# Kernel optimization log

Measured on AMD Instinct MI355X. Metric: run time of the kernel, lower is better.

The kernel has to match this reference:

```python
import jax, jax.numpy as jnp
import numpy as np
from jax import lax

B, T, N, D = 4, 12, 1024, 128
C_FRONT = 78           # front/back channel split used by the mixup
X_LAST = T // 2 - 1    # static row index of the last (only effective) mixup call
BS_ST = 6              # block_size of mixup_region_ST
SIGMA = 10.0
LN_EPS = 1e-5


def _mixup_region_ST(graph, y):
    """Faithful jax port of mixup_region_ST(graph_front, x=X_LAST, y, 6, sigma=10).
    graph: [T, N, C_FRONT] float; y: traced int scalar."""
    T_, N_, C_ = graph.shape
    x = X_LAST  # static python int
    y_start = jnp.maximum(y - BS_ST, 0)
    y_end = jnp.minimum(y + 2 * BS_ST, N_)

    # temporal gaussian mix of column y over rows [0, x), written at (x, y)
    xs = jnp.arange(x, dtype=graph.dtype)
    w = jnp.exp(-((xs - (x - 1.0)) ** 2) / (2.0 * SIGMA ** 2))
    w = w / w.sum()
    target = graph[:x, y, :]                      # [x, C]
    mixed_value = (w[:, None] * target).sum(0)    # [C]
    g = lax.dynamic_update_slice(graph, mixed_value[None, None, :], (x, y, 0))

    def mix_write(g_, bs, maxj):
        # average blocks g_[:, j*bs:(j+1)*bs, :] for j in [y_start//bs, y_end//bs)
        j0 = y_start // bs
        j1 = y_end // bs
        jj = jnp.arange(maxj)
        mask = (jj < (j1 - j0)).astype(g_.dtype)              # [maxj]
        cols = jnp.clip((j0 + jj)[:, None] * bs + jnp.arange(bs)[None, :], 0, N_ - 1)
        blocks = g_[:, cols, :]                               # [T, maxj, bs, C]
        mixed = (blocks * mask[None, :, None, None]).sum(1) / (j1 - j0).astype(g_.dtype)
        # torch writes mixed_region.to(torch.uint8) into a float tensor
        mixed = lax.stop_gradient(mixed.astype(jnp.uint8).astype(g_.dtype))
        return lax.dynamic_update_slice(g_, mixed, (0, y, 0))

    # torch resets block_size to 1 when y_end > w - block_size
    return lax.cond(y_end > N_ - BS_ST,
                    lambda g_: mix_write(g_, 1, 3 * BS_ST),
                    lambda g_: mix_write(g_, BS_ST, 4),
                    g)


def _forward(inp, adapt_G, xff_w, xff_b, ff1_w, ff1_b, ff2_w, ff2_b, ln_w, ln_b):
    x_ = inp @ xff_w.T + xff_b                       # [B,T,N,3D]
    q, k, v = jnp.split(x_, 3, axis=-1)
    e = jnp.einsum('btnd,btmd->btnm', q, k) / (D ** 0.5)
    e = e @ adapt_G                                  # [B,T,N,N]
    attn = jax.nn.softmax(e, axis=-1)
    attn_det = lax.stop_gradient(attn)               # self.attention_maps = attn.detach()

    def process(attn_b, val_b):                      # [T,N,N], [T,N,D]
        front = val_b[..., :C_FRONT]
        back = val_b[..., C_FRONT:]
        col_sums = attn_b.sum(axis=1)                # [T, N]
        _, idx = lax.top_k(-col_sums, 2)             # 2 smallest per row, ascending
        # only the last loop iteration's mixup survives in the original code
        y = idx[X_LAST, 1]
        return jnp.concatenate([_mixup_region_ST(front, y), back], axis=-1)

    new_value = jax.vmap(process)(attn_det, v)       # [B,T,N,D]
    vi = attn @ new_value                            # [B,T,N,D]
    h = jax.nn.gelu(vi @ ff1_w.T + ff1_b, approximate=False)
    h = h @ ff2_w.T + ff2_b
    out = h + inp
    mu = out.mean(-1, keepdims=True)
    var = ((out - mu) ** 2).mean(-1, keepdims=True)
    return (out - mu) / jnp.sqrt(var + LN_EPS) * ln_w + ln_b


def setup_inputs() -> dict:
    key = jax.random.key(0)
    ks = jax.random.split(key, 6)
    s = 0.02
    return {
        'input': jax.random.normal(ks[0], (B, T, N, D), jnp.float32),
        'adapt_G': jax.random.normal(ks[1], (N, N), jnp.float32) / np.float32(np.sqrt(N)),
        'xff_w': jax.random.normal(ks[2], (3 * D, D), jnp.float32) * s,
        'xff_b': jnp.zeros((3 * D,), jnp.float32),
        'ff1_w': jax.random.normal(ks[3], (D, D), jnp.float32) * s,
        'ff1_b': jnp.zeros((D,), jnp.float32),
        'ff2_w': jax.random.normal(ks[4], (D, D), jnp.float32) * s,
        'ff2_b': jnp.zeros((D,), jnp.float32),
        'ln_w': jnp.ones((D,), jnp.float32),
        'ln_b': jnp.zeros((D,), jnp.float32),
    }


def reference(input, adapt_G, xff_w, xff_b, ff1_w, ff1_b, ff2_w, ff2_b, ln_w, ln_b):
    return _forward(input, adapt_G, xff_w, xff_b, ff1_w, ff1_b, ff2_w, ff2_b, ln_w, ln_b)
```

## Files before the change

kernel.cpp:

```cpp
#include <hip/hip_runtime.h>
#include <hip/hip_bf16.h>

typedef __attribute__((ext_vector_type(8))) short bf16x8;
typedef __attribute__((ext_vector_type(4))) float f32x4;
typedef unsigned long long ull;

#define MFMA(a,b,c) __builtin_amdgcn_mfma_f32_16x16x32_bf16((a),(b),(c),0,0,0)
#define VMCNT(N) asm volatile("s_waitcnt vmcnt(%0)" :: "i"(N) : "memory")

__device__ __forceinline__ short f2bs(float f){
  union { float f; unsigned u; } x; x.f = f;
  unsigned r = (x.u + 0x7fffu + ((x.u >> 16) & 1u)) >> 16;
  return (short)r;
}
__device__ __forceinline__ float bs2f(short s){
  union { unsigned u; float f; } x; x.u = ((unsigned)(unsigned short)s) << 16;
  return x.f;
}

__device__ __forceinline__ void gl2lds16(const void* g, void* l){
  __builtin_amdgcn_global_load_lds((const __attribute__((address_space(1))) void*)g,
                                   (__attribute__((address_space(3))) void*)l, 16, 0, 0);
}

__device__ __forceinline__ void merge2(ull& a1, ull& a2, ull b1, ull b2){
  ull n1 = min(a1, b1);
  ull n2 = min(max(a1, b1), min(a2, b2));
  a1 = n1; a2 = n2;
}

__global__ void conv_kernel(const float* xffw, const float* w1, const float* w2,
                            short* wqkv_b, short* w1_b, short* w2_b){
  int i = blockIdx.x*blockDim.x + threadIdx.x;
  int stride = gridDim.x*blockDim.x;
  for (int idx = i; idx < 384*128; idx += stride) wqkv_b[idx] = f2bs(xffw[idx]);
  for (int idx = i; idx < 128*128; idx += stride) w1_b[idx] = f2bs(w1[idx]);
  for (int idx = i; idx < 128*128; idx += stride) w2_b[idx] = f2bs(w2[idx]);
}

__global__ __launch_bounds__(256) void gtrans_kernel(const float* __restrict__ G,
                                                     short* __restrict__ gt){
  __shared__ float tile[32][33];
  int bx = blockIdx.x & 31;
  int by = blockIdx.x >> 5;
  int tx = threadIdx.x & 31, ty = threadIdx.x >> 5;
  #pragma unroll
  for (int j=0;j<4;j++){
    int n = by*32 + ty + j*8;
    tile[ty+j*8][tx] = G[(size_t)n*1024 + bx*32 + tx];
  }
  __syncthreads();
  #pragma unroll
  for (int j=0;j<4;j++){
    int m = bx*32 + ty + j*8;
    gt[(size_t)m*1024 + by*32 + tx] = f2bs(tile[tx][ty+j*8]);
  }
}

__global__ __launch_bounds__(256,3) void qkv_kernel(const float* __restrict__ inp,
                                                  const short* __restrict__ wqkv,
                                                  const float* __restrict__ bias,
                                                  short* __restrict__ q, short* __restrict__ kT,
                                                  short* __restrict__ nvt){
  __shared__ __align__(16) char smem[49152];
  int w = threadIdx.x >> 6, lane = threadIdx.x & 63;
  int lr = lane & 15, lg = lane >> 4;
  int r0 = blockIdx.x*64;
  int bt = blockIdx.x >> 4;
  int n0 = r0 & 1023;
  int rw = r0 + w*16;
  bf16x8 a[4];
  #pragma unroll
  for (int kc=0;kc<4;kc++){
    const float* ar = inp + (size_t)(rw+lr)*128 + kc*32 + lg*8;
    float4 f0 = *(const float4*)ar;
    float4 f1 = *(const float4*)(ar+4);
    bf16x8 t;
    t[0]=f2bs(f0.x); t[1]=f2bs(f0.y); t[2]=f2bs(f0.z); t[3]=f2bs(f0.w);
    t[4]=f2bs(f1.x); t[5]=f2bs(f1.y); t[6]=f2bs(f1.z); t[7]=f2bs(f1.w);
    a[kc]=t;
  }
  auto stageW = [&](int buf, int kc){
    #pragma unroll
    for (int t=0;t<6;t++){
      int r = (w*6+t)*16 + (lane>>2);
      int s = (lane&3) ^ ((r>>1)&3);
      gl2lds16(wqkv + (size_t)r*128 + kc*32 + s*8,
               smem + buf*24576 + (w*6+t)*1024);
    }
  };
  f32x4 acc[24];
  #pragma unroll
  for (int j=0;j<24;j++) acc[j] = f32x4{0.f,0.f,0.f,0.f};
  stageW(0, 0);
  int cur = 0;
  for (int kc=0; kc<4; kc++){
    if (kc < 3) { stageW(cur^1, kc+1); VMCNT(6); } else { VMCNT(0); }
    __builtin_amdgcn_s_barrier();
    __builtin_amdgcn_sched_barrier(0);
    const char* wb = smem + cur*24576;
    #pragma unroll
    for (int jt=0;jt<24;jt++){
      int j = jt*16 + lr;
      bf16x8 b = *(const bf16x8*)(wb + (size_t)j*64 + ((lg ^ ((lr>>1)&3))*16));
      acc[jt] = MFMA(a[kc], b, acc[jt]);
    }
    __builtin_amdgcn_s_barrier();
    cur ^= 1;
  }
  #pragma unroll
  for (int jt=0;jt<8;jt++){
    float bj = bias[jt*16+lr];
    #pragma unroll
    for (int rr=0;rr<4;rr++)
      q[(size_t)(rw + lg*4 + rr)*128 + jt*16 + lr] = f2bs(acc[jt][rr] + bj);
  }
  __syncthreads();
  short (*tb)[72] = (short(*)[72])smem;
  #pragma unroll
  for (int jt=8;jt<16;jt++){
    int d = (jt-8)*16 + lr;
    float bj = bias[jt*16+lr];
    #pragma unroll
    for (int rr=0;rr<4;rr++) tb[d][w*16 + lg*4 + rr] = f2bs(acc[jt][rr] + bj);
  }
  __syncthreads();
  #pragma unroll
  for (int it=0;it<4;it++){
    int idx = it*256 + threadIdx.x;
    int row = idx >> 3, c8 = (idx & 7)*8;
    *(bf16x8*)(kT + ((size_t)bt*128 + row)*1024 + n0 + c8) = *(const bf16x8*)&tb[row][c8];
  }
  __syncthreads();
  #pragma unroll
  for (int jt=16;jt<24;jt++){
    int c = (jt-16)*16 + lr;
    float bj = bias[jt*16+lr];
    #pragma unroll
    for (int rr=0;rr<4;rr++) tb[c][w*16 + lg*4 + rr] = f2bs(acc[jt][rr] + bj);
  }
  __syncthreads();
  #pragma unroll
  for (int it=0;it<4;it++){
    int idx = it*256 + threadIdx.x;
    int row = idx >> 3, c8 = (idx & 7)*8;
    *(bf16x8*)(nvt + ((size_t)bt*128 + row)*1024 + n0 + c8) = *(const bf16x8*)&tb[row][c8];
  }
}

__global__ __launch_bounds__(256,3) void kg_kernel(const short* __restrict__ gt,
                                                   const short* __restrict__ kT,
                                                   short* __restrict__ kgt){
  __shared__ __align__(16) short gtl[2][64*64];
  __shared__ __align__(16) short ktl[2][128*64];
  int lb = (blockIdx.x & 7)*96 + (blockIdx.x >> 3);
  int bt = lb >> 4;
  int mt = lb & 15;
  int w = threadIdx.x>>6, lane = threadIdx.x&63, lr = lane&15, lg = lane>>4;
  int mblk = mt*64;
  const short* kbase = kT + (size_t)bt*128*1024;
  auto stage = [&](int b, int nc){
    int n0 = nc*64;
    #pragma unroll
    for (int t=0;t<2;t++){
      int row = w*16 + t*8 + (lane>>3);
      int cswz = ((lane&7)*16) ^ ((row&7)<<4);
      gl2lds16(gt + (size_t)(mblk+row)*1024 + n0 + (cswz>>1),
               (char*)gtl[b] + w*2048 + t*1024);
    }
    #pragma unroll
    for (int t=0;t<4;t++){
      int row = w*32 + t*8 + (lane>>3);
      int cswz = ((lane&7)*16) ^ ((row&7)<<4);
      gl2lds16(kbase + (size_t)row*1024 + n0 + (cswz>>1),
               (char*)ktl[b] + w*4096 + t*1024);
    }
  };
  f32x4 acc[8];
  #pragma unroll
  for (int i=0;i<8;i++) acc[i] = f32x4{0.f,0.f,0.f,0.f};
  stage(0, 0);
  int cur = 0;
  for (int nc=0; nc<16; nc++){
    if (nc < 15) { stage(cur^1, nc+1); VMCNT(6); } else { VMCNT(0); }
    __builtin_amdgcn_s_barrier();
    __builtin_amdgcn_sched_barrier(0);
    #pragma unroll
    for (int ks=0;ks<2;ks++){
      int arl = w*16 + lr;
      int acb = ks*64 + lg*16;
      bf16x8 af = *(const bf16x8*)((const char*)gtl[cur] + arl*128 + (acb ^ ((arl&7)<<4)));
      #pragma unroll
      for (int dt=0;dt<8;dt++){
        int brl = dt*16 + lr;
        bf16x8 bf = *(const bf16x8*)((const char*)ktl[cur] + brl*128 + (acb ^ ((brl&7)<<4)));
        acc[dt] = MFMA(af, bf, acc[dt]);
      }
    }
    __builtin_amdgcn_s_barrier();
    cur ^= 1;
  }
  const float SCALE = 0.08838834764831845f;
  int m = mblk + w*16 + lg*4;
  #pragma unroll
  for (int dt=0;dt<8;dt++){
    #pragma unroll
    for (int rr=0;rr<4;rr++){
      kgt[((size_t)(bt*1024 + m + rr))*128 + dt*16 + lr] = f2bs(acc[dt][rr]*SCALE);
    }
  }
}

__global__ __launch_bounds__(256,3) void fused_kernel(const short* __restrict__ q,
                                                      const short* __restrict__ kgt,
                                                      const short* __restrict__ nvt,
                                                      float* __restrict__ zbuf,
                                                      float* __restrict__ cspart,
                                                      short* __restrict__ vib){
  __shared__ __align__(16) short kgl[64*128];
  __shared__ __align__(16) short nvl[128*64];
  __shared__ __align__(16) short p_lds[4][16][68];
  __shared__ float csb[4][64];
  int lb = (blockIdx.x & 7)*96 + (blockIdx.x >> 3);
  int bt = lb >> 4;
  int rblk = lb & 15;
  int w = threadIdx.x>>6, lane = threadIdx.x&63, lr = lane&15, lg = lane>>4;
  int r0 = rblk*64 + w*16;
  const short* qrow = q + ((size_t)(bt*1024 + r0 + lr))*128;
  bf16x8 a[4];
  #pragma unroll
  for (int kc=0;kc<4;kc++) a[kc] = *(const bf16x8*)(qrow + kc*32 + lg*8);
  const short* kgb = kgt + (size_t)bt*1024*128;
  const short* nvb = nvt + (size_t)bt*128*1024;
  auto stage_kg = [&](int mc){
    int m0 = mc*64;
    #pragma unroll
    for (int t=0;t<4;t++){
      int row = w*16 + t*4 + (lane>>4);
      int cswz = ((lane&15)*16) ^ ((row&7)<<4);
      gl2lds16(kgb + (size_t)(m0+row)*128 + (cswz>>1),
               (char*)kgl + w*4096 + t*1024);
    }
  };
  auto stage_nv = [&](int mc){
    int m0 = mc*64;
    #pragma unroll
    for (int t=0;t<4;t++){
      int row = w*32 + t*8 + (lane>>3);
      int cswz = ((lane&7)*16) ^ ((row&7)<<4);
      gl2lds16(nvb + (size_t)row*1024 + m0 + (cswz>>1),
               (char*)nvl + w*4096 + t*1024);
    }
  };
  f32x4 acc[8];
  #pragma unroll
  for (int i=0;i<8;i++) acc[i] = f32x4{0.f,0.f,0.f,0.f};
  float zacc[4] = {0.f,0.f,0.f,0.f};
  for (int mc=0; mc<16; mc++){
    stage_kg(mc);
    stage_nv(mc);
    __syncthreads();
    #pragma unroll
    for (int s=0;s<4;s++){
      f32x4 e = f32x4{0.f,0.f,0.f,0.f};
      #pragma unroll
      for (int kc=0;kc<4;kc++){
        int rl = s*16 + lr;
        int cb = kc*64 + lg*16;
        bf16x8 kb = *(const bf16x8*)((const char*)kgl + rl*256 + (cb ^ ((rl&7)<<4)));
        e = MFMA(a[kc], kb, e);
      }
      #pragma unroll
      for (int rr=0;rr<4;rr++){
        float p = __expf(fminf(e[rr], 60.f));
        zacc[rr] += p;
        p_lds[w][lg*4+rr][s*16+lr] = f2bs(p);
      }
    }
    bf16x8 pa0 = *(const bf16x8*)&p_lds[w][lr][lg*8];
    bf16x8 pa1 = *(const bf16x8*)&p_lds[w][lr][32+lg*8];
    #pragma unroll
    for (int ct=0; ct<8; ct++){
      int c = ct*16 + lr;
      int mb0 = lg*16;
      int mb1 = 64 + lg*16;
      bf16x8 nb0 = *(const bf16x8*)((const char*)nvl + c*128 + (mb0 ^ ((c&7)<<4)));
      bf16x8 nb1 = *(const bf16x8*)((const char*)nvl + c*128 + (mb1 ^ ((c&7)<<4)));
      acc[ct] = MFMA(pa0, nb0, acc[ct]);
      acc[ct] = MFMA(pa1, nb1, acc[ct]);
    }
    __syncthreads();
  }
  #pragma unroll
  for (int d=1;d<16;d<<=1){
    #pragma unroll
    for (int rr=0;rr<4;rr++) zacc[rr] += __shfl_xor(zacc[rr], d, 64);
  }
  if (lr==0){
    #pragma unroll
    for (int rr=0;rr<4;rr++) zbuf[(size_t)bt*1024 + r0 + lg*4 + rr] = zacc[rr];
  }
  float inv[4];
  #pragma unroll
  for (int rr=0;rr<4;rr++) inv[rr] = 1.0f/zacc[rr];
  #pragma unroll
  for (int ct=0;ct<8;ct++){
    #pragma unroll
    for (int rr=0;rr<4;rr++){
      vib[((size_t)(bt*1024 + r0 + lg*4 + rr))*128 + ct*16 + lr] = f2bs(acc[ct][rr]*inv[rr]);
    }
  }
  int t5 = bt % 12, b = bt / 12;
  if (t5 == 5){
    for (int mc=0; mc<16; mc++){
      stage_kg(mc);
      __syncthreads();
      int m0 = mc*64;
      float cs[4];
      #pragma unroll
      for (int s=0;s<4;s++){
        f32x4 e = f32x4{0.f,0.f,0.f,0.f};
        #pragma unroll
        for (int kc=0;kc<4;kc++){
          int rl = s*16 + lr;
          int cb = kc*64 + lg*16;
          bf16x8 kb = *(const bf16x8*)((const char*)kgl + rl*256 + (cb ^ ((rl&7)<<4)));
          e = MFMA(a[kc], kb, e);
        }
        float c = 0.f;
        #pragma unroll
        for (int rr=0;rr<4;rr++) c += __expf(fminf(e[rr],60.f))*inv[rr];
        c += __shfl_xor(c, 16, 64);
        c += __shfl_xor(c, 32, 64);
        cs[s] = c;
      }
      if (lg==0){
        #pragma unroll
        for (int s=0;s<4;s++) csb[w][s*16+lr] = cs[s];
      }
      __syncthreads();
      if (w==0){
        int j = lane;
        float tot = csb[0][j]+csb[1][j]+csb[2][j]+csb[3][j];
        cspart[((size_t)(b*16 + rblk))*1024 + m0 + j] = tot;
      }
    }
  }
}

__global__ __launch_bounds__(256) void top2_kernel(const float* __restrict__ cspart,
                                                   int* __restrict__ yidx){
  __shared__ ull s1[4], s2[4];
  int b = blockIdx.x;
  ull b1 = ~0ull, b2 = ~0ull;
  #pragma unroll
  for (int j=0;j<4;j++){
    int col = j*256 + threadIdx.x;
    float s = 0.f;
    #pragma unroll
    for (int blk=0;blk<16;blk++) s += cspart[((size_t)(b*16 + blk))*1024 + col];
    union { float f; unsigned u; } cv; cv.f = s;
    ull key = ((ull)cv.u << 32) | (unsigned)col;
    merge2(b1, b2, key, ~0ull);
  }
  #pragma unroll
  for (int d=1;d<64;d<<=1){
    ull o1 = __shfl_xor(b1, d, 64);
    ull o2 = __shfl_xor(b2, d, 64);
    merge2(b1, b2, o1, o2);
  }
  int w = threadIdx.x >> 6;
  if ((threadIdx.x & 63) == 0){ s1[w] = b1; s2[w] = b2; }
  __syncthreads();
  if (threadIdx.x == 0){
    ull r1 = s1[0], r2 = s2[0];
    merge2(r1, r2, s1[1], s2[1]);
    merge2(r1, r2, s1[2], s2[2]);
    merge2(r1, r2, s1[3], s2[3]);
    yidx[b] = (int)(r2 & 0xffffffffu);
  }
}

__global__ void nvfixA_kernel(const short* __restrict__ nvt, const int* __restrict__ yidx,
                              float* __restrict__ mixres){
  int bt = blockIdx.x; int b = bt/12, t = bt%12;
  int y = yidx[b];
  int y_start = max(y-6, 0), y_end = min(y+12, 1024);
  int bs, j0, cnt;
  if (y_end > 1024-6){ bs = 1; j0 = y_start; cnt = y_end - y_start; }
  else { bs = 6; j0 = y_start/6; cnt = y_end/6 - j0; }
  int items = bs*78;
  int idx = threadIdx.x;
  if (idx >= items) return;
  int i = idx / 78, c = idx % 78;
  const short* nvb = nvt + (size_t)bt*128*1024;
  float acc = 0.f;
  for (int jj=0;jj<cnt;jj++){
    int col = (j0+jj)*bs + i;
    float gv;
    if (t == 5 && col == y){
      float wsum = 0.f, mv = 0.f;
      #pragma unroll
      for (int tp=0;tp<5;tp++){
        float d = (float)tp - 4.0f;
        float w = __expf(-d*d/200.0f);
        wsum += w;
        mv += w * bs2f(nvt[((size_t)(b*12+tp)*128 + c)*1024 + y]);
      }
      gv = mv / wsum;
    } else {
      gv = bs2f(nvb[(size_t)c*1024 + col]);
    }
    acc += gv;
  }
  mixres[((size_t)bt*6 + i)*78 + c] = acc / (float)cnt;
}

__global__ __launch_bounds__(256) void corr_kernel(const short* __restrict__ q,
                                                   const short* __restrict__ kgt,
                                                   const short* __restrict__ nvt,
                                                   const float* __restrict__ mixres,
                                                   const float* __restrict__ zbuf,
                                                   const int* __restrict__ yidx,
                                                   short* __restrict__ vib){
  __shared__ __align__(16) short kcol[6][128];
  __shared__ float delta[6][78];
  int bt = blockIdx.x >> 2;
  int rc = blockIdx.x & 3;
  int b = bt/12;
  int y = yidx[b];
  int y_end = min(y+12, 1024);
  int bs = (y_end > 1024-6) ? 1 : 6;
  for (int idx = threadIdx.x; idx < 6*128; idx += 256){
    int i = idx >> 7, d = idx & 127;
    kcol[i][d] = (i < bs) ? kgt[((size_t)(bt*1024 + y + i))*128 + d] : (short)0;
  }
  for (int idx = threadIdx.x; idx < 6*78; idx += 256){
    int i = idx / 78, c = idx % 78;
    float dv = 0.f;
    if (i < bs){
      float avg = mixres[((size_t)bt*6 + i)*78 + c];
      int ti = (int)avg;
      unsigned char u = (unsigned char)ti;
      dv = (float)u - bs2f(nvt[((size_t)bt*128 + c)*1024 + (y+i)]);
    }
    delta[i][c] = dv;
  }
  __syncthreads();
  int r = rc*256 + threadIdx.x;
  const short* qr = q + ((size_t)(bt*1024 + r))*128;
  float e[6] = {0.f,0.f,0.f,0.f,0.f,0.f};
  for (int d0 = 0; d0 < 128; d0 += 8){
    bf16x8 qv = *(const bf16x8*)(qr + d0);
    #pragma unroll
    for (int j=0;j<8;j++){
      float qf = bs2f(qv[j]);
      #pragma unroll
      for (int i=0;i<6;i++) e[i] += qf * bs2f(kcol[i][d0+j]);
    }
  }
  float invz = 1.0f / zbuf[(size_t)bt*1024 + r];
  float p[6];
  #pragma unroll
  for (int i=0;i<6;i++) p[i] = (i < bs) ? __expf(fminf(e[i],60.f))*invz : 0.f;
  short* vr = vib + ((size_t)(bt*1024 + r))*128;
  for (int c=0;c<78;c++){
    float dsum = 0.f;
    #pragma unroll
    for (int i=0;i<6;i++) dsum += p[i]*delta[i][c];
    vr[c] = f2bs(bs2f(vr[c]) + dsum);
  }
}

__global__ __launch_bounds__(256,3) void ffn_kernel(const short* __restrict__ vib,
                                                  const float* __restrict__ inp,
                                                  const short* __restrict__ w1b,
                                                  const short* __restrict__ w2b,
                                                  const float* __restrict__ b1,
                                                  const float* __restrict__ b2,
                                                  const float* __restrict__ lnw,
                                                  const float* __restrict__ lnb,
                                                  float* __restrict__ out){
  __shared__ __align__(16) short wl[128*128];
  __shared__ __align__(16) short h_lds[4][16][72];
  int w = threadIdx.x>>6, lane = threadIdx.x&63, lr = lane&15, lg = lane>>4;
  int r0 = blockIdx.x*64 + w*16;
  auto stageW = [&](const short* src){
    #pragma unroll
    for (int t=0;t<8;t++){
      int r = (w*8+t)*4 + (lane>>4);
      int s = (lane&15) ^ (r&7);
      gl2lds16(src + (size_t)r*128 + s*8, (char*)wl + (w*8+t)*1024);
    }
  };
  stageW(w1b);
  bf16x8 a[4];
  #pragma unroll
  for (int kc=0;kc<4;kc++) a[kc] = *(const bf16x8*)(vib + (size_t)(r0+lr)*128 + kc*32 + lg*8);
  __syncthreads();
  f32x4 acc[8];
  #pragma unroll
  for (int i=0;i<8;i++) acc[i] = f32x4{0.f,0.f,0.f,0.f};
  #pragma unroll
  for (int kc=0;kc<4;kc++){
    #pragma unroll
    for (int jt=0;jt<8;jt++){
      bf16x8 b = *(const bf16x8*)((const char*)wl + (size_t)(jt*16+lr)*256 + (((kc*4+lg) ^ (lr&7))*16));
      acc[jt] = MFMA(a[kc], b, acc[jt]);
    }
  }
  #pragma unroll
  for (int jt=0;jt<8;jt++){
    float bj = b1[jt*16+lr];
    #pragma unroll
    for (int rr=0;rr<4;rr++){
      float x = acc[jt][rr] + bj;
      float g = 0.5f*x*(1.0f + erff(x*0.70710678118654752f));
      h_lds[w][lg*4+rr][jt*16+lr] = f2bs(g);
    }
  }
  __syncthreads();
  stageW(w2b);
  bf16x8 ha[4];
  #pragma unroll
  for (int kc=0;kc<4;kc++) ha[kc] = *(const bf16x8*)&h_lds[w][lr][kc*32 + lg*8];
  __syncthreads();
  f32x4 acc2[8];
  #pragma unroll
  for (int i=0;i<8;i++) acc2[i] = f32x4{0.f,0.f,0.f,0.f};
  #pragma unroll
  for (int kc=0;kc<4;kc++){
    #pragma unroll
    for (int jt=0;jt<8;jt++){
      bf16x8 b = *(const bf16x8*)((const char*)wl + (size_t)(jt*16+lr)*256 + (((kc*4+lg) ^ (lr&7))*16));
      acc2[jt] = MFMA(ha[kc], b, acc2[jt]);
    }
  }
  float xv[8][4];
  #pragma unroll
  for (int jt=0;jt<8;jt++){
    float bj = b2[jt*16+lr];
    #pragma unroll
    for (int rr=0;rr<4;rr++){
      xv[jt][rr] = acc2[jt][rr] + bj + inp[(size_t)(r0 + lg*4 + rr)*128 + jt*16 + lr];
    }
  }
  float mu[4], rstd[4];
  #pragma unroll
  for (int rr=0;rr<4;rr++){
    float s = 0.f;
    #pragma unroll
    for (int jt=0;jt<8;jt++) s += xv[jt][rr];
    #pragma unroll
    for (int m=1;m<16;m<<=1) s += __shfl_xor(s, m, 64);
    mu[rr] = s * (1.0f/128.0f);
  }
  #pragma unroll
  for (int rr=0;rr<4;rr++){
    float s = 0.f;
    #pragma unroll
    for (int jt=0;jt<8;jt++){ float d = xv[jt][rr]-mu[rr]; s += d*d; }
    #pragma unroll
    for (int m=1;m<16;m<<=1) s += __shfl_xor(s, m, 64);
    rstd[rr] = rsqrtf(s * (1.0f/128.0f) + 1e-5f);
  }
  #pragma unroll
  for (int jt=0;jt<8;jt++){
    int col = jt*16 + lr;
    float lw = lnw[col], lb = lnb[col];
    #pragma unroll
    for (int rr=0;rr<4;rr++){
      out[(size_t)(r0 + lg*4 + rr)*128 + col] = (xv[jt][rr]-mu[rr])*rstd[rr]*lw + lb;
    }
  }
}

extern "C" void kernel_launch(void* const* d_in, const int* in_sizes, int n_in,
                              void* d_out, int out_size, void* d_ws, size_t ws_size,
                              hipStream_t stream) {
  (void)in_sizes; (void)n_in; (void)out_size;
  const float* inp  = (const float*)d_in[0];
  const float* G    = (const float*)d_in[1];
  const float* xffw = (const float*)d_in[2];
  const float* xffb = (const float*)d_in[3];
  const float* w1   = (const float*)d_in[4];
  const float* b1   = (const float*)d_in[5];
  const float* w2   = (const float*)d_in[6];
  const float* b2   = (const float*)d_in[7];
  const float* lnw  = (const float*)d_in[8];
  const float* lnb  = (const float*)d_in[9];
  float* out = (float*)d_out;
  char* ws = (char*)d_ws;

  size_t off = 0;
  auto take = [&](size_t bytes)->char*{ char* p = ws + off; off += (bytes + 255) & ~(size_t)255; return p; };
  short* wqkv_b = (short*)take(384*128*2);
  short* gt_b   = (short*)take((size_t)1024*1024*2);
  short* w1_b   = (short*)take(128*128*2);
  short* w2_b   = (short*)take(128*128*2);
  short* qb     = (short*)take((size_t)48*1024*128*2);
  short* kTb    = (short*)take((size_t)48*128*1024*2);
  short* nvt    = (short*)take((size_t)48*128*1024*2);
  short* kgt    = (short*)take((size_t)48*1024*128*2);
  float* zbuf   = (float*)take((size_t)48*1024*4);
  float* cspart = (float*)take((size_t)4*16*1024*4);
  int*   yidx   = (int*)take(256);
  float* mixres = (float*)take((size_t)48*6*78*4);
  short* vibuf  = (short*)take((size_t)48*1024*128*2);
  if (off > ws_size) return;

  conv_kernel<<<dim3(32), dim3(256), 0, stream>>>(xffw, w1, w2, wqkv_b, w1_b, w2_b);
  gtrans_kernel<<<dim3(1024), dim3(256), 0, stream>>>(G, gt_b);
  qkv_kernel<<<dim3(768), dim3(256), 0, stream>>>(inp, wqkv_b, xffb, qb, kTb, nvt);
  kg_kernel<<<dim3(768), dim3(256), 0, stream>>>(gt_b, kTb, kgt);
  fused_kernel<<<dim3(768), dim3(256), 0, stream>>>(qb, kgt, nvt, zbuf, cspart, vibuf);
  top2_kernel<<<dim3(4), dim3(256), 0, stream>>>(cspart, yidx);
  nvfixA_kernel<<<dim3(48), dim3(512), 0, stream>>>(nvt, yidx, mixres);
  corr_kernel<<<dim3(192), dim3(256), 0, stream>>>(qb, kgt, nvt, mixres, zbuf, yidx, vibuf);
  ffn_kernel<<<dim3(768), dim3(256), 0, stream>>>(vibuf, inp, w1_b, w2_b, b1, b2, lnw, lnb, out);
}
```

Baseline: 160.2 us.

## Prefetch next K/V tiles in fused attention and offload column sums via stored probabilities

The fused attention loop now prefetches the next kg tile during the softmax phase and the next nv tile during the PV MFMA phase, using explicit vmcnt waits and raw barriers instead of a synchronous load then __syncthreads. The second pass over K for the t==5 slices, which recomputed exp scores to build column sums, is removed. Instead those blocks write their bf16 probability tiles to a buffer, and a new colsum kernel reduces them with 1/z normalisation before top2. This removes the serialised tail on 64 of the 768 blocks, at the cost of an extra launch, an 8MB write and read, and bf16 rounding of the column sums.

```diff
diff --git a/kernel.cpp b/kernel.cpp
--- a/kernel.cpp
+++ b/kernel.cpp
@@ -215,17 +215,18 @@
                                                       const short* __restrict__ kgt,
                                                       const short* __restrict__ nvt,
                                                       float* __restrict__ zbuf,
-                                                      float* __restrict__ cspart,
+                                                      short* __restrict__ pbuf,
                                                       short* __restrict__ vib){
   __shared__ __align__(16) short kgl[64*128];
   __shared__ __align__(16) short nvl[128*64];
-  __shared__ __align__(16) short p_lds[4][16][68];
-  __shared__ float csb[4][64];
+  __shared__ __align__(16) short p_lds[4][16][72];
   int lb = (blockIdx.x & 7)*96 + (blockIdx.x >> 3);
   int bt = lb >> 4;
   int rblk = lb & 15;
   int w = threadIdx.x>>6, lane = threadIdx.x&63, lr = lane&15, lg = lane>>4;
   int r0 = rblk*64 + w*16;
+  bool is5 = (bt % 12) == 5;
+  int bq = bt / 12;
   const short* qrow = q + ((size_t)(bt*1024 + r0 + lr))*128;
   bf16x8 a[4];
   #pragma unroll
@@ -256,10 +257,13 @@
   #pragma unroll
   for (int i=0;i<8;i++) acc[i] = f32x4{0.f,0.f,0.f,0.f};
   float zacc[4] = {0.f,0.f,0.f,0.f};
+  stage_kg(0);
+  stage_nv(0);
+  VMCNT(0);
+  __builtin_amdgcn_s_barrier();
+  __builtin_amdgcn_sched_barrier(0);
   for (int mc=0; mc<16; mc++){
-    stage_kg(mc);
-    stage_nv(mc);
-    __syncthreads();
+    int m0 = mc*64;
     #pragma unroll
     for (int s=0;s<4;s++){
       f32x4 e = f32x4{0.f,0.f,0.f,0.f};
@@ -277,6 +281,11 @@
         p_lds[w][lg*4+rr][s*16+lr] = f2bs(p);
       }
     }
+    __builtin_amdgcn_s_barrier();
+    if (mc < 15) stage_kg(mc+1);
+    if (mc < 15) { VMCNT(4); } else { VMCNT(0); }
+    __builtin_amdgcn_s_barrier();
+    __builtin_amdgcn_sched_barrier(0);
     bf16x8 pa0 = *(const bf16x8*)&p_lds[w][lr][lg*8];
     bf16x8 pa1 = *(const bf16x8*)&p_lds[w][lr][32+lg*8];
     #pragma unroll
@@ -289,7 +298,19 @@
       acc[ct] = MFMA(pa0, nb0, acc[ct]);
       acc[ct] = MFMA(pa1, nb1, acc[ct]);
     }
-    __syncthreads();
+    if (is5){
+      #pragma unroll
+      for (int tt=0; tt<4; tt++){
+        int row = tt*4 + (lane>>4);
+        int m = (lane&15)*4;
+        ull v = *(const ull*)&p_lds[w][row][m];
+        *(ull*)(pbuf + ((size_t)bq*1024 + r0 + row)*1024 + m0 + m) = v;
+      }
+    }
+    __builtin_amdgcn_s_barrier();
+    if (mc < 15) { stage_nv(mc+1); VMCNT(4); } else { VMCNT(0); }
+    __builtin_amdgcn_s_barrier();
+    __builtin_amdgcn_sched_barrier(0);
   }
   #pragma unroll
   for (int d=1;d<16;d<<=1){
@@ -310,45 +331,31 @@
       vib[((size_t)(bt*1024 + r0 + lg*4 + rr))*128 + ct*16 + lr] = f2bs(acc[ct][rr]*inv[rr]);
     }
   }
-  int t5 = bt % 12, b = bt / 12;
-  if (t5 == 5){
-    for (int mc=0; mc<16; mc++){
-      stage_kg(mc);
-      __syncthreads();
-      int m0 = mc*64;
-      float cs[4];
-      #pragma unroll
-      for (int s=0;s<4;s++){
-        f32x4 e = f32x4{0.f,0.f,0.f,0.f};
-        #pragma unroll
-        for (int kc=0;kc<4;kc++){
-          int rl = s*16 + lr;
-          int cb = kc*64 + lg*16;
-          bf16x8 kb = *(const bf16x8*)((const char*)kgl + rl*256 + (cb ^ ((rl&7)<<4)));
-          e = MFMA(a[kc], kb, e);
-        }
-        float c = 0.f;
-        #pragma unroll
-        for (int rr=0;rr<4;rr++) c += __expf(fminf(e[rr],60.f))*inv[rr];
-        c += __shfl_xor(c, 16, 64);
-        c += __shfl_xor(c, 32, 64);
-        cs[s] = c;
-      }
-      if (lg==0){
-        #pragma unroll
-        for (int s=0;s<4;s++) csb[w][s*16+lr] = cs[s];
-      }
-      __syncthreads();
-      if (w==0){
-        int j = lane;
-        float tot = csb[0][j]+csb[1][j]+csb[2][j]+csb[3][j];
-        cspart[((size_t)(b*16 + rblk))*1024 + m0 + j] = tot;
-      }
-    }
-  }
-}
-
-__global__ __launch_bounds__(256) void top2_kernel(const float* __restrict__ cspart,
+}
+
+__global__ __launch_bounds__(256) void colsum_kernel(const short* __restrict__ pbuf,
+                                                     const float* __restrict__ zbuf,
+                                                     float* __restrict__ csfinal){
+  __shared__ float part[4][64];
+  int b = blockIdx.x >> 4, mg = blockIdx.x & 15;
+  int t = threadIdx.x;
+  int mcol = mg*64 + (t & 63);
+  int rq = t >> 6;
+  const short* pb = pbuf + (size_t)b*1024*1024;
+  const float* zb = zbuf + (size_t)(b*12 + 5)*1024;
+  float s = 0.f;
+  for (int r = rq*256; r < rq*256 + 256; r++){
+    s += bs2f(pb[(size_t)r*1024 + mcol]) * (1.0f/zb[r]);
+  }
+  part[rq][t & 63] = s;
+  __syncthreads();
+  if (t < 64){
+    float cs = (part[0][t] + part[1][t]) + (part[2][t] + part[3][t]);
+    csfinal[(size_t)b*1024 + mg*64 + t] = cs;
+  }
+}
+
+__global__ __launch_bounds__(256) void top2_kernel(const float* __restrict__ csfinal,
                                                    int* __restrict__ yidx){
   __shared__ ull s1[4], s2[4];
   int b = blockIdx.x;
@@ -356,9 +363,7 @@
   #pragma unroll
   for (int j=0;j<4;j++){
     int col = j*256 + threadIdx.x;
-    float s = 0.f;
-    #pragma unroll
-    for (int blk=0;blk<16;blk++) s += cspart[((size_t)(b*16 + blk))*1024 + col];
+    float s = csfinal[(size_t)b*1024 + col];
     union { float f; unsigned u; } cv; cv.f = s;
     ull key = ((ull)cv.u << 32) | (unsigned)col;
     merge2(b1, b2, key, ~0ull);
@@ -603,7 +608,8 @@
   short* nvt    = (short*)take((size_t)48*128*1024*2);
   short* kgt    = (short*)take((size_t)48*1024*128*2);
   float* zbuf   = (float*)take((size_t)48*1024*4);
-  float* cspart = (float*)take((size_t)4*16*1024*4);
+  short* pbuf   = (short*)take((size_t)4*1024*1024*2);
+  float* csfin  = (float*)take((size_t)4*1024*4);
   int*   yidx   = (int*)take(256);
   float* mixres = (float*)take((size_t)48*6*78*4);
   short* vibuf  = (short*)take((size_t)48*1024*128*2);
@@ -613,8 +619,9 @@
   gtrans_kernel<<<dim3(1024), dim3(256), 0, stream>>>(G, gt_b);
   qkv_kernel<<<dim3(768), dim3(256), 0, stream>>>(inp, wqkv_b, xffb, qb, kTb, nvt);
   kg_kernel<<<dim3(768), dim3(256), 0, stream>>>(gt_b, kTb, kgt);
-  fused_kernel<<<dim3(768), dim3(256), 0, stream>>>(qb, kgt, nvt, zbuf, cspart, vibuf);
-  top2_kernel<<<dim3(4), dim3(256), 0, stream>>>(cspart, yidx);
+  fused_kernel<<<dim3(768), dim3(256), 0, stream>>>(qb, kgt, nvt, zbuf, pbuf, vibuf);
+  colsum_kernel<<<dim3(64), dim3(256), 0, stream>>>(pbuf, zbuf, csfin);
+  top2_kernel<<<dim3(4), dim3(256), 0, stream>>>(csfin, yidx);
   nvfixA_kernel<<<dim3(48), dim3(512), 0, stream>>>(nvt, yidx, mixres);
   corr_kernel<<<dim3(192), dim3(256), 0, stream>>>(qb, kgt, nvt, mixres, zbuf, yidx, vibuf);
   ffn_kernel<<<dim3(768), dim3(256), 0, stream>>>(vibuf, inp, w1_b, w2_b, b1, b2, lnw, lnb, out);
```

Measured after the change: 157.1 us. No clear change (-1.9%).
